# Performance work log

Hardware: AMD Instinct MI355X
Metric: run time of the kernel (lower is better)

## Reference

```python
import jax, jax.numpy as jnp
import numpy as np

B, C, H, W = 8, 128, 48, 48
RED = 16  # SELayer reduction


def setup_inputs() -> dict:
    key = jax.random.key(0)
    ks = jax.random.split(key, 8)
    s = 0.05  # weight scale for numerical stability of softmax
    return {
        "x": jax.random.normal(ks[0], (B, C, H, W), jnp.float32),
        "Wq": jax.random.normal(ks[1], (C, C), jnp.float32) * s,
        "bq": jnp.zeros((C,), jnp.float32),
        "Wk": jax.random.normal(ks[2], (C, C), jnp.float32) * s,
        "bk": jnp.zeros((C,), jnp.float32),
        "Wv": jax.random.normal(ks[3], (C, C), jnp.float32) * s,
        "bv": jnp.zeros((C,), jnp.float32),
        "se_w1": jax.random.normal(ks[4], (C // RED, C), jnp.float32) * s,
        "se_w2": jax.random.normal(ks[5], (C, C // RED), jnp.float32) * s,
        "gamma": jax.random.normal(ks[6], (1,), jnp.float32),
    }


def reference(x, Wq, bq, Wk, bk, Wv, bv, se_w1, se_w2, gamma):
    b, c, h, w = x.shape
    n = h * w
    xf = x.reshape(b, c, n)  # (B, C, N)
    # 1x1 convs == per-pixel linear maps over channels
    q = jnp.einsum('oc,bcn->bon', Wq, xf) + bq[None, :, None]  # (B, C, N)
    k = jnp.einsum('oc,bcn->bon', Wk, xf) + bk[None, :, None]
    v = jnp.einsum('oc,bcn->bon', Wv, xf) + bv[None, :, None]
    # energy[b, i, j] = sum_c q[b, c, i] * k[b, c, j]  (unscaled, as in source)
    energy = jnp.einsum('bci,bcj->bij', q, k)  # (B, N, N)
    attn = jax.nn.softmax(energy, axis=-1)
    # out[b, c, i] = sum_j v[b, c, j] * attn[b, i, j]
    out = jnp.einsum('bcj,bij->bci', v, attn).reshape(b, c, h, w)
    # SELayer applied to the input x
    y = jnp.mean(x, axis=(2, 3))  # (B, C) global average pool
    y = jax.nn.relu(y @ se_w1.T)  # (B, C//RED)
    y = jax.nn.sigmoid(y @ se_w2.T)  # (B, C)
    x_se = x * y[:, :, None, None]
    return gamma[0] * out + x_se
```

## Files before the change

### kernel.cpp

```cpp
#include <hip/hip_runtime.h>

typedef _Float16 half8 __attribute__((ext_vector_type(8)));
typedef _Float16 half4 __attribute__((ext_vector_type(4)));
typedef float f32x4 __attribute__((ext_vector_type(4)));

#define BATCH 8
#define CH 128
#define NPIX 2304
#define SPLIT 4
#define JPER (NPIX / SPLIT)
#define BN (BATCH * NPIX)
#define LOG2E 1.44269504088896f

__device__ __forceinline__ f32x4 mfma32(half8 a, half8 b, f32x4 c) {
    return __builtin_amdgcn_mfma_f32_16x16x32_f16(a, b, c, 0, 0, 0);
}
__device__ __forceinline__ f32x4 mfma16(half4 a, half4 b, f32x4 c) {
    return __builtin_amdgcn_mfma_f32_16x16x16f16(a, b, c, 0, 0, 0);
}

__global__ __launch_bounds__(256) void k_prep(
        const float* __restrict__ x, const float* __restrict__ Wq,
        const float* __restrict__ Wk, const float* __restrict__ Wv,
        _Float16* __restrict__ Wh, float* __restrict__ y0) {
    const int bid = blockIdx.x;
    const int t = threadIdx.x;
    if (bid < 1024) {
        const int row = bid;
        const float4* p = (const float4*)(x + (size_t)row * NPIX);
        float s = 0.f;
        for (int tt = t; tt < NPIX / 4; tt += 256) {
            float4 v = p[tt];
            s += v.x + v.y + v.z + v.w;
        }
        for (int m = 1; m < 64; m <<= 1) s += __shfl_xor(s, m);
        __shared__ float ls[4];
        if ((t & 63) == 0) ls[t >> 6] = s;
        __syncthreads();
        if (t == 0) y0[row] = (ls[0] + ls[1] + ls[2] + ls[3]) * (1.0f / (float)NPIX);
    } else {
        int i = (bid - 1024) * 256 + t;
        const float* src = (i < 16384) ? Wq : ((i < 32768) ? Wk : Wv);
        Wh[i] = (_Float16)src[i & 16383];
    }
}

__global__ __launch_bounds__(256) void k_proj(
        const float* __restrict__ x, const _Float16* __restrict__ Wh,
        const float* __restrict__ bq, const float* __restrict__ bk, const float* __restrict__ bv,
        _Float16* __restrict__ qT, _Float16* __restrict__ kT, _Float16* __restrict__ vN,
        const float* __restrict__ y0, const float* __restrict__ se_w1,
        const float* __restrict__ se_w2, float* __restrict__ scale) {
    const int which = blockIdx.z;
    const int t = threadIdx.x;

    if (which == 3) {
        if (blockIdx.x != 0 || blockIdx.y != 0) return;
        __shared__ float ly[128];
        __shared__ float ly1[8];
        for (int b = 0; b < BATCH; ++b) {
            if (t < 128) ly[t] = y0[b * 128 + t];
            __syncthreads();
            if (t < 8) {
                float a = 0.f;
                for (int c = 0; c < 128; ++c) a += se_w1[t * 128 + c] * ly[c];
                ly1[t] = fmaxf(a, 0.f);
            }
            __syncthreads();
            if (t < 128) {
                float a = 0.f;
                for (int r = 0; r < 8; ++r) a += se_w2[t * 8 + r] * ly1[r];
                scale[b * 128 + t] = 1.f / (1.f + __expf(-a));
            }
            __syncthreads();
        }
        return;
    }

    const int n0 = blockIdx.x * 128;
    const int b = blockIdx.y;
    const float* bias = (which == 0) ? bq : ((which == 1) ? bk : bv);
    const _Float16* W = Wh + which * 16384;

    __shared__ __align__(16) _Float16 xt[128 * 128];

    {
        const float* xb = x + (size_t)b * CH * NPIX + n0;
        for (int rep = 0; rep < 16; ++rep) {
            int flat = rep * 256 + t;
            int c = flat >> 5;
            int n4 = (flat & 31) * 4;
            float4 v4 = *(const float4*)(xb + (size_t)c * NPIX + n4);
            int cc = c & 7, ck = c >> 3;
            xt[(n4 + 0) * 128 + ((ck ^ ((n4 + 0) & 7)) * 8) + cc] = (_Float16)v4.x;
            xt[(n4 + 1) * 128 + ((ck ^ ((n4 + 1) & 7)) * 8) + cc] = (_Float16)v4.y;
            xt[(n4 + 2) * 128 + ((ck ^ ((n4 + 2) & 7)) * 8) + cc] = (_Float16)v4.z;
            xt[(n4 + 3) * 128 + ((ck ^ ((n4 + 3) & 7)) * 8) + cc] = (_Float16)v4.w;
        }
    }
    __syncthreads();

    const int lane = t & 63, w = t >> 6;
    const int ln15 = lane & 15, quad = lane >> 4;

    f32x4 zero4 = {0.f, 0.f, 0.f, 0.f};
    f32x4 acc[8][2];
    for (int mt = 0; mt < 8; ++mt) { acc[mt][0] = zero4; acc[mt][1] = zero4; }

    for (int ks = 0; ks < 4; ++ks) {
        half8 bf[2];
        for (int nt = 0; nt < 2; ++nt) {
            int row = w * 32 + nt * 16 + ln15;
            int ch = ks * 4 + quad;
            bf[nt] = *(const half8*)(xt + row * 128 + ((ch ^ (row & 7)) * 8));
        }
        for (int mt = 0; mt < 8; ++mt) {
            half8 af = *(const half8*)(W + (mt * 16 + ln15) * 128 + ks * 32 + quad * 8);
            acc[mt][0] = mfma32(af, bf[0], acc[mt][0]);
            acc[mt][1] = mfma32(af, bf[1], acc[mt][1]);
        }
    }
    __syncthreads();

    if (which == 2) {
        for (int mt = 0; mt < 8; ++mt)
            for (int nt = 0; nt < 2; ++nt)
                for (int r = 0; r < 4; ++r) {
                    int c = mt * 16 + quad * 4 + r;
                    int nl = w * 32 + nt * 16 + ln15;
                    xt[c * 128 + (((nl >> 3) ^ (c & 7)) * 8) + (nl & 7)] =
                        (_Float16)(acc[mt][nt][r] + bias[c]);
                }
        __syncthreads();
        _Float16* vb = vN + (size_t)b * CH * NPIX + n0;
        for (int rep = 0; rep < 8; ++rep) {
            int c = rep * 16 + (t >> 4), ch = t & 15;
            *(half8*)(vb + (size_t)c * NPIX + ch * 8) =
                *(const half8*)(xt + c * 128 + ((ch ^ (c & 7)) * 8));
        }
    } else {
        for (int mt = 0; mt < 8; ++mt)
            for (int nt = 0; nt < 2; ++nt)
                for (int r = 0; r < 4; ++r) {
                    int c = mt * 16 + quad * 4 + r;
                    int nl = w * 32 + nt * 16 + ln15;
                    xt[nl * 128 + (((c >> 3) ^ (nl & 7)) * 8) + (c & 7)] =
                        (_Float16)(acc[mt][nt][r] + bias[c]);
                }
        __syncthreads();
        _Float16* dst = ((which == 0) ? qT : kT) + ((size_t)b * NPIX + n0) * CH;
        for (int rep = 0; rep < 8; ++rep) {
            int nl = rep * 16 + (t >> 4), ch = t & 15;
            *(half8*)(dst + nl * 128 + ch * 8) =
                *(const half8*)(xt + nl * 128 + ((ch ^ (nl & 7)) * 8));
        }
    }
}

__global__ __launch_bounds__(256, 4) void k_attn(
        const _Float16* __restrict__ qT, const _Float16* __restrict__ kT,
        const _Float16* __restrict__ vN,
        _Float16* __restrict__ o_part, float* __restrict__ g_m, float* __restrict__ g_l) {
    const int i0 = blockIdx.x * 64;
    const int b = blockIdx.y;
    const int split = blockIdx.z;
    const int t = threadIdx.x;
    const int lane = t & 63, w = t >> 6;
    const int ln15 = lane & 15, quad = lane >> 4;

    __shared__ __align__(16) _Float16 sh[16384];
    _Float16* k_s = sh;
    _Float16* v_s = sh + 8192;

    half8 qf[4];
    {
        const _Float16* qb = qT + ((size_t)b * NPIX + i0 + w * 16 + ln15) * CH + quad * 8;
        for (int kc = 0; kc < 4; ++kc) qf[kc] = *(const half8*)(qb + kc * 32);
    }

    const int krow = t >> 4;
    const int kch  = t & 15;
    const int vco  = t >> 3;
    const int vch  = t & 7;
    const _Float16* kb0 = kT + ((size_t)b * NPIX) * CH;
    const _Float16* vb0 = vN + (size_t)b * CH * NPIX;

    half8 kr[4], vr[4];
    {
        const int j0 = split * JPER;
        const _Float16* kb = kb0 + (size_t)(j0 + krow) * CH + kch * 8;
        for (int r = 0; r < 4; ++r) kr[r] = *(const half8*)(kb + (size_t)(r * 16) * CH);
        const _Float16* vb = vb0 + j0 + vch * 8;
        for (int r = 0; r < 4; ++r) vr[r] = *(const half8*)(vb + (size_t)(r * 32 + vco) * NPIX);
    }

    f32x4 zero4 = {0.f, 0.f, 0.f, 0.f};
    f32x4 os[8];
    for (int ct = 0; ct < 8; ++ct) os[ct] = zero4;
    float m = -1e30f, l = 0.f;

    for (int it = 0; it < 9; ++it) {
        __syncthreads();

        {
            for (int r = 0; r < 4; ++r) {
                int row = r * 16 + krow;
                *(half8*)(k_s + row * 128 + ((kch ^ (row & 7)) * 8)) = kr[r];
            }
            for (int r = 0; r < 4; ++r) {
                int c = r * 32 + vco;
                *(half8*)(v_s + c * 64 + ((vch ^ (c & 7)) * 8)) = vr[r];
            }
        }
        if (it < 8) {
            const int j0n = split * JPER + (it + 1) * 64;
            const _Float16* kb = kb0 + (size_t)(j0n + krow) * CH + kch * 8;
            for (int r = 0; r < 4; ++r) kr[r] = *(const half8*)(kb + (size_t)(r * 16) * CH);
            const _Float16* vb = vb0 + j0n + vch * 8;
            for (int r = 0; r < 4; ++r) vr[r] = *(const half8*)(vb + (size_t)(r * 32 + vco) * NPIX);
        }
        asm volatile("s_waitcnt lgkmcnt(0)" ::: "memory");
        asm volatile("s_barrier" ::: "memory");

        f32x4 s[4];
        for (int jt = 0; jt < 4; ++jt) s[jt] = zero4;
        __builtin_amdgcn_s_setprio(1);
        for (int jt = 0; jt < 4; ++jt) {
            for (int kc = 0; kc < 4; ++kc) {
                int row = jt * 16 + ln15, ch = kc * 4 + quad;
                half8 kf = *(const half8*)(k_s + row * 128 + ((ch ^ (row & 7)) * 8));
                s[jt] = mfma32(kf, qf[kc], s[jt]);
            }
        }
        __builtin_amdgcn_s_setprio(0);

        float mx = fmaxf(fmaxf(s[0][0], s[0][1]), fmaxf(s[0][2], s[0][3]));
        for (int jt = 1; jt < 4; ++jt)
            mx = fmaxf(mx, fmaxf(fmaxf(s[jt][0], s[jt][1]), fmaxf(s[jt][2], s[jt][3])));
        mx = fmaxf(mx, __shfl_xor(mx, 16));
        mx = fmaxf(mx, __shfl_xor(mx, 32));
        if (!__all(mx - m <= 8.0f)) {
            float mnew = fmaxf(m, mx);
            float alpha = exp2f((m - mnew) * LOG2E);
            for (int ct = 0; ct < 8; ++ct) {
                os[ct][0] *= alpha; os[ct][1] *= alpha;
                os[ct][2] *= alpha; os[ct][3] *= alpha;
            }
            l *= alpha;
            m = mnew;
        }
        float mbias = m * LOG2E;

        float sum = 0.f;
        half4 pf[4];
        for (int jt = 0; jt < 4; ++jt)
            for (int r = 0; r < 4; ++r) {
                float p = exp2f(fmaf(s[jt][r], LOG2E, -mbias));
                sum += p;
                pf[jt][r] = (_Float16)p;
            }
        sum += __shfl_xor(sum, 16);
        sum += __shfl_xor(sum, 32);
        l += sum;

        __builtin_amdgcn_s_setprio(1);
        for (int ct = 0; ct < 8; ++ct) {
            int c = ct * 16 + ln15;
            for (int jt = 0; jt < 4; ++jt) {
                int chunk = jt * 2 + (quad >> 1);
                half4 vf = *(const half4*)(v_s + c * 64 + ((chunk ^ (c & 7)) * 8) + (quad & 1) * 4);
                os[ct] = mfma16(vf, pf[jt], os[ct]);
            }
        }
        __builtin_amdgcn_s_setprio(0);
    }

    if (quad == 0) {
        int i = i0 + w * 16 + ln15;
        g_m[(size_t)(split * BATCH + b) * NPIX + i] = m;
        g_l[(size_t)(split * BATCH + b) * NPIX + i] = l;
    }
    const float linv = 1.0f / l;
    __syncthreads();
    for (int ct = 0; ct < 8; ++ct)
        for (int r = 0; r < 4; ++r) {
            int c = ct * 16 + quad * 4 + r;
            int il = w * 16 + ln15;
            int chunk = (il >> 3);
            sh[c * 64 + ((chunk ^ (c & 7)) * 8) + (il & 7)] = (_Float16)(os[ct][r] * linv);
        }
    __syncthreads();
    _Float16* op = o_part + (size_t)(split * BATCH + b) * CH * NPIX;
    for (int rep = 0; rep < 4; ++rep) {
        int c = rep * 32 + (t >> 3), ch = t & 7;
        *(half8*)(op + (size_t)c * NPIX + i0 + ch * 8) =
            *(const half8*)(sh + c * 64 + ((ch ^ (c & 7)) * 8));
    }
}

__global__ __launch_bounds__(256) void k_combine(
        const _Float16* __restrict__ o_part, const float* __restrict__ g_m,
        const float* __restrict__ g_l, const float* __restrict__ x,
        const float* __restrict__ scale, const float* __restrict__ gamma_p,
        float* __restrict__ out) {
    const int i0 = blockIdx.x * 64;
    const int b = blockIdx.y;
    const int t = threadIdx.x;
    __shared__ float wl[SPLIT][64];

    if (t < 64) {
        int i = i0 + t;
        float mm[SPLIT], llv[SPLIT];
        float M = -1e30f;
        for (int s = 0; s < SPLIT; ++s) {
            mm[s] = g_m[(size_t)(s * BATCH + b) * NPIX + i];
            llv[s] = g_l[(size_t)(s * BATCH + b) * NPIX + i];
            M = fmaxf(M, mm[s]);
        }
        float L = 0.f, e[SPLIT];
        for (int s = 0; s < SPLIT; ++s) {
            e[s] = exp2f((mm[s] - M) * LOG2E);
            L += e[s] * llv[s];
        }
        float inv = 1.f / L;
        for (int s = 0; s < SPLIT; ++s) wl[s][t] = e[s] * llv[s] * inv;
    }
    __syncthreads();

    const float g = gamma_p[0];
    for (int rep = 0; rep < 4; ++rep) {
        int c = rep * 32 + (t >> 3), i8 = (t & 7) * 8;
        size_t base = ((size_t)b * CH + c) * NPIX + i0 + i8;
        float acc[8] = {0.f, 0.f, 0.f, 0.f, 0.f, 0.f, 0.f, 0.f};
        for (int s = 0; s < SPLIT; ++s) {
            half8 o = *(const half8*)(o_part +
                ((size_t)(s * BATCH + b) * CH + c) * NPIX + i0 + i8);
            for (int e = 0; e < 8; ++e) acc[e] += wl[s][i8 + e] * (float)o[e];
        }
        float sc = scale[b * 128 + c];
        float4 x0 = *(const float4*)(x + base);
        float4 x1 = *(const float4*)(x + base + 4);
        float4 r0, r1;
        r0.x = g * acc[0] + x0.x * sc; r0.y = g * acc[1] + x0.y * sc;
        r0.z = g * acc[2] + x0.z * sc; r0.w = g * acc[3] + x0.w * sc;
        r1.x = g * acc[4] + x1.x * sc; r1.y = g * acc[5] + x1.y * sc;
        r1.z = g * acc[6] + x1.z * sc; r1.w = g * acc[7] + x1.w * sc;
        *(float4*)(out + base) = r0;
        *(float4*)(out + base + 4) = r1;
    }
}

extern "C" void kernel_launch(void* const* d_in, const int* in_sizes, int n_in,
                              void* d_out, int out_size, void* d_ws, size_t ws_size,
                              hipStream_t stream) {
    const float* x     = (const float*)d_in[0];
    const float* Wq    = (const float*)d_in[1];
    const float* bq    = (const float*)d_in[2];
    const float* Wk    = (const float*)d_in[3];
    const float* bk    = (const float*)d_in[4];
    const float* Wv    = (const float*)d_in[5];
    const float* bv    = (const float*)d_in[6];
    const float* se_w1 = (const float*)d_in[7];
    const float* se_w2 = (const float*)d_in[8];
    const float* gamma = (const float*)d_in[9];
    float* out = (float*)d_out;

    char* ws = (char*)d_ws;
    const size_t E = (size_t)BATCH * NPIX * CH;
    _Float16* qT = (_Float16*)(ws);
    _Float16* kT = (_Float16*)(ws + E * 2);
    _Float16* vN = (_Float16*)(ws + E * 4);
    _Float16* op = (_Float16*)(ws + E * 6);
    char* tail   = ws + E * 6 + (size_t)SPLIT * E * 2;
    _Float16* Wh = (_Float16*)(tail);
    float* g_m   = (float*)(tail + 98304);
    float* g_l   = (float*)(tail + 98304 + SPLIT * BN * 4);
    float* y0    = (float*)(tail + 98304 + 2 * SPLIT * BN * 4);
    float* scale = (float*)(tail + 98304 + 2 * SPLIT * BN * 4 + 4096);

    k_prep<<<1216, 256, 0, stream>>>(x, Wq, Wk, Wv, Wh, y0);
    k_proj<<<dim3(NPIX / 128, BATCH, 4), 256, 0, stream>>>(
        x, Wh, bq, bk, bv, qT, kT, vN, y0, se_w1, se_w2, scale);
    k_attn<<<dim3(NPIX / 64, BATCH, SPLIT), 256, 0, stream>>>(
        qT, kT, vN, op, g_m, g_l);
    k_combine<<<dim3(NPIX / 64, BATCH), 256, 0, stream>>>(
        op, g_m, g_l, x, scale, gamma, out);
}
```

Baseline: 172.2 us.

## Stage K/V tiles with direct global-to-LDS loads into double-buffered shared memory

The attention kernel no longer pulls K and V tiles through registers and then writes them into LDS. It now issues global_load_lds transfers straight into a second LDS buffer while the current buffer is being consumed, and applies the XOR swizzle on the global-address side. This is meant to free the staging registers and the LDS-write instructions and to overlap loading the next tile with the MFMA work. In exchange, LDS use per block doubles to 64KB and the occupancy hint drops from 4 to 2 blocks. The loop now also depends on the end-of-iteration barrier waiting for the outstanding DMA loads to finish.

```diff
diff --git a/kernel.cpp b/kernel.cpp
--- a/kernel.cpp
+++ b/kernel.cpp
@@ -17,6 +17,12 @@
 }
 __device__ __forceinline__ f32x4 mfma16(half4 a, half4 b, f32x4 c) {
     return __builtin_amdgcn_mfma_f32_16x16x16f16(a, b, c, 0, 0, 0);
+}
+
+__device__ __forceinline__ void gl_lds16(const _Float16* g, _Float16* l) {
+    typedef const __attribute__((address_space(1))) unsigned int gu32;
+    typedef __attribute__((address_space(3))) unsigned int lu32;
+    __builtin_amdgcn_global_load_lds((gu32*)g, (lu32*)l, 16, 0, 0);
 }
 
 __global__ __launch_bounds__(256) void k_prep(
@@ -157,7 +163,7 @@
     }
 }
 
-__global__ __launch_bounds__(256, 4) void k_attn(
+__global__ __launch_bounds__(256, 2) void k_attn(
         const _Float16* __restrict__ qT, const _Float16* __restrict__ kT,
         const _Float16* __restrict__ vN,
         _Float16* __restrict__ o_part, float* __restrict__ g_m, float* __restrict__ g_l) {
@@ -168,9 +174,7 @@
     const int lane = t & 63, w = t >> 6;
     const int ln15 = lane & 15, quad = lane >> 4;
 
-    __shared__ __align__(16) _Float16 sh[16384];
-    _Float16* k_s = sh;
-    _Float16* v_s = sh + 8192;
+    __shared__ __align__(16) _Float16 sh[32768];
 
     half8 qf[4];
     {
@@ -178,49 +182,42 @@
         for (int kc = 0; kc < 4; ++kc) qf[kc] = *(const half8*)(qb + kc * 32);
     }
 
-    const int krow = t >> 4;
-    const int kch  = t & 15;
-    const int vco  = t >> 3;
-    const int vch  = t & 7;
     const _Float16* kb0 = kT + ((size_t)b * NPIX) * CH;
     const _Float16* vb0 = vN + (size_t)b * CH * NPIX;
 
-    half8 kr[4], vr[4];
-    {
-        const int j0 = split * JPER;
-        const _Float16* kb = kb0 + (size_t)(j0 + krow) * CH + kch * 8;
-        for (int r = 0; r < 4; ++r) kr[r] = *(const half8*)(kb + (size_t)(r * 16) * CH);
-        const _Float16* vb = vb0 + j0 + vch * 8;
-        for (int r = 0; r < 4; ++r) vr[r] = *(const half8*)(vb + (size_t)(r * 32 + vco) * NPIX);
-    }
+    auto stage = [&](int j0, _Float16* buf) {
+        #pragma unroll
+        for (int r = 0; r < 4; ++r) {
+            int idx = r * 4 + w;
+            int row = 4 * idx + (lane >> 4);
+            int ch  = (lane & 15) ^ (row & 7);
+            gl_lds16(kb0 + (size_t)(j0 + row) * CH + ch * 8,
+                     buf + idx * 512);
+        }
+        #pragma unroll
+        for (int r = 0; r < 4; ++r) {
+            int idx = r * 4 + w;
+            int c  = 8 * idx + (lane >> 3);
+            int ch = (lane & 7) ^ (c & 7);
+            gl_lds16(vb0 + (size_t)c * NPIX + j0 + ch * 8,
+                     buf + 8192 + idx * 512);
+        }
+    };
+
+    stage(split * JPER, sh);
+    __syncthreads();
 
     f32x4 zero4 = {0.f, 0.f, 0.f, 0.f};
     f32x4 os[8];
     for (int ct = 0; ct < 8; ++ct) os[ct] = zero4;
     float m = -1e30f, l = 0.f;
+    int cur = 0;
 
     for (int it = 0; it < 9; ++it) {
-        __syncthreads();
-
-        {
-            for (int r = 0; r < 4; ++r) {
-                int row = r * 16 + krow;
-                *(half8*)(k_s + row * 128 + ((kch ^ (row & 7)) * 8)) = kr[r];
-            }
-            for (int r = 0; r < 4; ++r) {
-                int c = r * 32 + vco;
-                *(half8*)(v_s + c * 64 + ((vch ^ (c & 7)) * 8)) = vr[r];
-            }
-        }
-        if (it < 8) {
-            const int j0n = split * JPER + (it + 1) * 64;
-            const _Float16* kb = kb0 + (size_t)(j0n + krow) * CH + kch * 8;
-            for (int r = 0; r < 4; ++r) kr[r] = *(const half8*)(kb + (size_t)(r * 16) * CH);
-            const _Float16* vb = vb0 + j0n + vch * 8;
-            for (int r = 0; r < 4; ++r) vr[r] = *(const half8*)(vb + (size_t)(r * 32 + vco) * NPIX);
-        }
-        asm volatile("s_waitcnt lgkmcnt(0)" ::: "memory");
-        asm volatile("s_barrier" ::: "memory");
+        _Float16* k_s = sh + cur * 16384;
+        _Float16* v_s = k_s + 8192;
+
+        if (it < 8) stage(split * JPER + (it + 1) * 64, sh + (cur ^ 1) * 16384);
 
         f32x4 s[4];
         for (int jt = 0; jt < 4; ++jt) s[jt] = zero4;
@@ -273,6 +270,9 @@
             }
         }
         __builtin_amdgcn_s_setprio(0);
+
+        __syncthreads();
+        cur ^= 1;
     }
 
     if (quad == 0) {
@@ -281,7 +281,6 @@
         g_l[(size_t)(split * BATCH + b) * NPIX + i] = l;
     }
     const float linv = 1.0f / l;
-    __syncthreads();
     for (int ct = 0; ct < 8; ++ct)
         for (int r = 0; r < 4; ++r) {
             int c = ct * 16 + quad * 4 + r;
```

New measurement: 162.9 us. 1.06x faster.
